# Performance work log

Hardware: AMD Instinct MI355X
Metric: run time of the kernel (lower is better)

The kernel has to match this reference:

```python
import jax, jax.numpy as jnp
import numpy as np

D, VH, DFF, NL, VOCAB, NH, NKV, HD, R, SCALE = 4096, 1024, 14336, 2, 32000, 32, 8, 128, 8, 4.0
B, NIMG, T = 2, 257, 511
S = NIMG + T

def _rmsnorm(x, w, eps=1e-5):
    v = jnp.mean(jnp.square(x), axis=-1, keepdims=True)
    return x * jax.lax.rsqrt(v + eps) * w

def _lora(x, W, A, Bm):
    # base (dequantized NF4 equivalent) matmul + low-rank LoRA path, scaling = alpha/r
    base = jnp.einsum('...d,od->...o', x, W)
    low = jnp.einsum('...r,or->...o', jnp.einsum('...d,rd->...r', x, A), Bm)
    return base + low * SCALE

def _rope_tables(s):
    inv = 1.0 / (10000.0 ** (jnp.arange(0, HD, 2, dtype=jnp.float32) / HD))
    ang = jnp.arange(s, dtype=jnp.float32)[:, None] * inv[None, :]
    c, sn = jnp.cos(ang), jnp.sin(ang)
    return jnp.concatenate([c, c], -1), jnp.concatenate([sn, sn], -1)

def _apply_rope(x, cos, sin):
    rot = jnp.concatenate([-x[..., HD // 2:], x[..., :HD // 2]], -1)
    return x * cos + rot * sin

def _forward(image_embeds, proj_W, proj_b, embed, ln1, ln2, ln_f, Wq, Aq, Bq, Wk, Ak, Bk, Wv, Av, Bv, Wo, Ao, Bo, Wg, Ag, Bg, Wu, Au, Bu, Wd, Ad, Bd, input_ids, attention_mask):
    b = image_embeds.shape[0]
    img = jnp.einsum('bsv,dv->bsd', image_embeds, proj_W) + proj_b  # projector
    txt = embed[input_ids]                                          # token embedding lookup
    h = jnp.concatenate([img, txt], axis=1)                         # (B, S, D)
    s = h.shape[1]
    cos, sin = _rope_tables(s)
    allow = jnp.tril(jnp.ones((s, s), bool))[None, None] & (attention_mask[:, None, None, :] > 0)
    for i in range(NL):
        x = _rmsnorm(h, ln1[i])
        q = _lora(x, Wq[i], Aq[i], Bq[i]).reshape(b, s, NH, HD).transpose(0, 2, 1, 3)
        k = _lora(x, Wk[i], Ak[i], Bk[i]).reshape(b, s, NKV, HD).transpose(0, 2, 1, 3)
        v = _lora(x, Wv[i], Av[i], Bv[i]).reshape(b, s, NKV, HD).transpose(0, 2, 1, 3)
        q = _apply_rope(q, cos, sin)
        k = _apply_rope(k, cos, sin)
        k = jnp.repeat(k, NH // NKV, axis=1)  # GQA: expand kv heads
        v = jnp.repeat(v, NH // NKV, axis=1)
        scores = jnp.einsum('bhsd,bhtd->bhst', q, k) / jnp.sqrt(jnp.float32(HD))
        scores = jnp.where(allow, scores, jnp.float32(-1e30))
        attn = jnp.einsum('bhst,bhtd->bhsd', jax.nn.softmax(scores, axis=-1), v)
        attn = attn.transpose(0, 2, 1, 3).reshape(b, s, D)
        h = h + _lora(attn, Wo[i], Ao[i], Bo[i])
        x = _rmsnorm(h, ln2[i])
        h = h + _lora(jax.nn.silu(_lora(x, Wg[i], Ag[i], Bg[i])) * _lora(x, Wu[i], Au[i], Bu[i]), Wd[i], Ad[i], Bd[i])
    return _rmsnorm(h, ln_f)  # HF hidden_states[-1] is post final norm

def setup_inputs():
    key = jax.random.key(0)
    ks = iter(jax.random.split(key, 40))
    n = lambda shape, sc=0.02: jax.random.normal(next(ks), shape, jnp.float32) * sc
    return dict(
        image_embeds=jax.random.normal(next(ks), (B, NIMG, VH), jnp.float32),
        input_ids=jax.random.randint(next(ks), (B, T), 0, VOCAB),
        attention_mask=jnp.ones((B, S), jnp.int32),
        proj_W=n((D, VH)), proj_b=jnp.zeros((D,), jnp.float32),
        embed=n((VOCAB, D)),
        ln1=jnp.ones((NL, D), jnp.float32), ln2=jnp.ones((NL, D), jnp.float32), ln_f=jnp.ones((D,), jnp.float32),
        Wq=n((NL, D, D)), Aq=n((NL, R, D)), Bq=n((NL, D, R)),
        Wk=n((NL, NKV * HD, D)), Ak=n((NL, R, D)), Bk=n((NL, NKV * HD, R)),
        Wv=n((NL, NKV * HD, D)), Av=n((NL, R, D)), Bv=n((NL, NKV * HD, R)),
        Wo=n((NL, D, D)), Ao=n((NL, R, D)), Bo=n((NL, D, R)),
        Wg=n((NL, DFF, D)), Ag=n((NL, R, D)), Bg=n((NL, DFF, R)),
        Wu=n((NL, DFF, D)), Au=n((NL, R, D)), Bu=n((NL, DFF, R)),
        Wd=n((NL, D, DFF)), Ad=n((NL, R, DFF)), Bd=n((NL, D, R)),
    )

def reference(image_embeds, input_ids, attention_mask, proj_W, proj_b, embed, ln1, ln2, ln_f, Wq, Aq, Bq, Wk, Ak, Bk, Wv, Av, Bv, Wo, Ao, Bo, Wg, Ag, Bg, Wu, Au, Bu, Wd, Ad, Bd):
    return _forward(image_embeds, proj_W, proj_b, embed, ln1, ln2, ln_f, Wq, Aq, Bq, Wk, Ak, Bk, Wv, Av, Bv, Wo, Ao, Bo, Wg, Ag, Bg, Wu, Au, Bu, Wd, Ad, Bd, input_ids, attention_mask)
```

## Files before the change

kernel.cpp:

```cpp
#include <hip/hip_runtime.h>
#include <hip/hip_bf16.h>
#include <cstdint>
#include <cstddef>

typedef unsigned short u16;
typedef unsigned int u32;
typedef __attribute__((ext_vector_type(8))) short short8;
typedef __attribute__((ext_vector_type(4))) short short4v;
typedef __attribute__((ext_vector_type(4))) float f32x4;

__device__ __forceinline__ u16 f2bf(float f) {
  u32 u = __float_as_uint(f);
  u32 r = (u + 0x7FFFu + ((u >> 16) & 1u)) >> 16;
  return (u16)r;
}
__device__ __forceinline__ float bf2f(u16 u) {
  return __uint_as_float(((u32)u) << 16);
}
__device__ __forceinline__ short f2bf_hw(float f) {
  union { __hip_bfloat16 h; u16 u; } c;
  c.h = __float2bfloat16(f);
  return (short)c.u;
}

__device__ __forceinline__ void gload_lds16(const void* g, void* l) {
  __builtin_amdgcn_global_load_lds((const __attribute__((address_space(1))) void*)g,
                                   (__attribute__((address_space(3))) void*)l, 16, 0, 0);
}

__global__ __launch_bounds__(256) void convert_w_kernel(const float* __restrict__ src,
    u16* __restrict__ dst, long n8) {
  long stride = (long)gridDim.x * 256;
  for (long i = (long)blockIdx.x * 256 + threadIdx.x; i < n8; i += stride) {
    const float* p = src + i * 8;
    float4 v0 = *(const float4*)p;
    float4 v1 = *(const float4*)(p + 4);
    uint4 w;
    w.x = (u32)(u16)f2bf_hw(v0.x) | ((u32)(u16)f2bf_hw(v0.y) << 16);
    w.y = (u32)(u16)f2bf_hw(v0.z) | ((u32)(u16)f2bf_hw(v0.w) << 16);
    w.z = (u32)(u16)f2bf_hw(v1.x) | ((u32)(u16)f2bf_hw(v1.y) << 16);
    w.w = (u32)(u16)f2bf_hw(v1.z) | ((u32)(u16)f2bf_hw(v1.w) << 16);
    *(uint4*)(dst + i * 8) = w;
  }
}

struct ConvJob { const float* src; u16* dst; long n8; };
struct GemmArgs {
  const u16* A; int M; int K; int lda;
  const float* W0; const float* LB0; int toff0;
  const float* W1; const float* LB1; int toff1;
  const float* W2; const float* LB2; int toff2;
  const u16* Wb0; const u16* Wb1; const u16* Wb2;
  int ldw;
  int seg1; int seg2;
  const float* t;
  const float* bias;
  const float* resid;
  float* outf; int ostride;
  u16* outb0; u16* outb1;
  int rowremap;
  float* outp;
  int ny_main;
  ConvJob cj[3];
};

template<int WMODE>
__global__ __launch_bounds__(256) void gemm_kernel(GemmArgs a) {
  __shared__ u16 Asm[128 * 64];
  __shared__ u16 BsmW[WMODE ? 128 * 64 : 128 * 128];
  const int tid = threadIdx.x;

  const int nconv = (int)gridDim.y - a.ny_main;
  if ((int)blockIdx.y < nconv) {
    if (blockIdx.z != 0) return;
    const long cb = (long)blockIdx.y * gridDim.x + blockIdx.x;
    const long cstr = (long)nconv * gridDim.x * 256;
#pragma unroll
    for (int j = 0; j < 3; j++) {
      const float* src = a.cj[j].src;
      if (!src) break;
      u16* dst = a.cj[j].dst;
      const long n8 = a.cj[j].n8;
      for (long i = cb * 256 + tid; i < n8; i += cstr) {
        const float* p = src + i * 8;
        float4 v0 = *(const float4*)p;
        float4 v1 = *(const float4*)(p + 4);
        uint4 w;
        w.x = (u32)(u16)f2bf_hw(v0.x) | ((u32)(u16)f2bf_hw(v0.y) << 16);
        w.y = (u32)(u16)f2bf_hw(v0.z) | ((u32)(u16)f2bf_hw(v0.w) << 16);
        w.z = (u32)(u16)f2bf_hw(v1.x) | ((u32)(u16)f2bf_hw(v1.y) << 16);
        w.w = (u32)(u16)f2bf_hw(v1.z) | ((u32)(u16)f2bf_hw(v1.w) << 16);
        *(uint4*)(dst + i * 8) = w;
      }
    }
    return;
  }
  const int yid = (int)blockIdx.y - nconv;

  const int nwg = gridDim.x * a.ny_main;
  const int bid0 = yid * gridDim.x + blockIdx.x;
  const int q = nwg >> 3, r = nwg & 7;
  const int xcd = bid0 & 7, pos = bid0 >> 3;
  const int nb = (xcd < r ? xcd * (q + 1) : r * (q + 1) + (xcd - r) * q) + pos;
  const int m0 = (nb % gridDim.x) * 128;
  const int n0 = (nb / gridDim.x) * 128;

  const float* W = a.W0; const u16* Wb = a.Wb0;
  const float* LB = a.LB0; int toff = a.toff0; int nbase = 0;
  if (a.seg2 && n0 >= a.seg2)      { W = a.W2; Wb = a.Wb2; LB = a.LB2; toff = a.toff2; nbase = a.seg2; }
  else if (a.seg1 && n0 >= a.seg1) { W = a.W1; Wb = a.Wb1; LB = a.LB1; toff = a.toff1; nbase = a.seg1; }
  const int koff = blockIdx.z * a.K;
  const u16* Ab = a.A + koff;
  const float* Wt = W + (size_t)(n0 - nbase) * a.ldw + koff;
  const u16* Wbt = Wb + (size_t)(n0 - nbase) * a.ldw + koff;

  const int lane = tid & 63, wid = tid >> 6;
  const int wr = wid >> 1, wcn = wid & 1;
  const int lrow = lane & 15, g = lane >> 4;
  const int arow = lane >> 3;
  const int aslot = (lane & 7) ^ arow;
  const int brow4 = lane >> 4;

  f32x4 acc[4][4] = {};

  auto dma_A = [&](int k0) {
#pragma unroll
    for (int i = 0; i < 4; i++) {
      int c = wid * 4 + i;
      const u16* src = Ab + (size_t)(m0 + c * 8 + arow) * a.lda + k0 + (aslot << 3);
      gload_lds16(src, &Asm[c * 512]);
    }
  };
  auto dma_B = [&](int k0) {
    if (WMODE) {
#pragma unroll
      for (int i = 0; i < 4; i++) {
        int c = wid * 4 + i;
        const u16* src = Wbt + (size_t)(c * 8 + arow) * a.ldw + k0 + (aslot << 3);
        gload_lds16(src, &BsmW[c * 512]);
      }
    } else {
      float* Bf = (float*)BsmW;
#pragma unroll
      for (int j = 0; j < 8; j++) {
        int rrow = wid * 32 + j * 4 + brow4;
        int sslot = (lane & 15) ^ (rrow & 7);
        const float* src = Wt + (size_t)rrow * a.ldw + k0 + (sslot << 2);
        gload_lds16(src, &Bf[(wid * 32 + j * 4) * 64]);
      }
    }
  };

  dma_A(0);
  dma_B(0);
  const int nk = a.K >> 6;
  for (int kt = 0; kt < nk; kt++) {
    __syncthreads();

    short8 af[4][2], bq[4][2];
#pragma unroll
    for (int mi = 0; mi < 4; mi++) {
      int row = wr * 64 + mi * 16 + lrow;
#pragma unroll
      for (int x = 0; x < 2; x++) {
        int s = x * 4 + g;
        af[mi][x] = *(const short8*)&Asm[row * 64 + ((s ^ (lrow & 7)) << 3)];
      }
    }
#pragma unroll
    for (int ni = 0; ni < 4; ni++) {
      int row = wcn * 64 + ni * 16 + lrow;
      if (WMODE) {
#pragma unroll
        for (int x = 0; x < 2; x++) {
          int s = x * 4 + g;
          bq[ni][x] = *(const short8*)&BsmW[row * 64 + ((s ^ (lrow & 7)) << 3)];
        }
      } else {
        const float* bp = (const float*)BsmW + row * 64;
        int m = row & 7;
#pragma unroll
        for (int x = 0; x < 2; x++) {
          int sg0 = x * 8 + g * 2;
          f32x4 lo = *(const f32x4*)(bp + ((sg0 ^ m) << 2));
          f32x4 hi = *(const f32x4*)(bp + (((sg0 + 1) ^ m) << 2));
          short8 sv;
          sv[0] = f2bf_hw(lo[0]); sv[1] = f2bf_hw(lo[1]);
          sv[2] = f2bf_hw(lo[2]); sv[3] = f2bf_hw(lo[3]);
          sv[4] = f2bf_hw(hi[0]); sv[5] = f2bf_hw(hi[1]);
          sv[6] = f2bf_hw(hi[2]); sv[7] = f2bf_hw(hi[3]);
          bq[ni][x] = sv;
        }
      }
    }

    asm volatile("s_waitcnt lgkmcnt(0)" ::: "memory");
    __builtin_amdgcn_sched_barrier(0);
    __builtin_amdgcn_s_barrier();
    __builtin_amdgcn_sched_barrier(0);
    if (kt + 1 < nk) {
      dma_A((kt + 1) << 6);
      dma_B((kt + 1) << 6);
    }
#pragma unroll
    for (int x = 0; x < 2; x++)
#pragma unroll
      for (int mi = 0; mi < 4; mi++)
#pragma unroll
        for (int ni = 0; ni < 4; ni++)
          acc[mi][ni] = __builtin_amdgcn_mfma_f32_16x16x32_bf16(af[mi][x], bq[ni][x], acc[mi][ni], 0, 0, 0);
  }

  if (a.outp) {
    float* op = a.outp + (size_t)blockIdx.z * (1536 * 4096);
#pragma unroll
    for (int mi = 0; mi < 4; mi++)
#pragma unroll
      for (int rr = 0; rr < 4; rr++) {
        int row = m0 + wr * 64 + mi * 16 + (g << 2) + rr;
#pragma unroll
        for (int ni = 0; ni < 4; ni++) {
          int n = n0 + wcn * 64 + ni * 16 + lrow;
          op[(size_t)row * a.ostride + n] = acc[mi][ni][rr];
        }
      }
    return;
  }
  const bool dolora = (a.t != nullptr);
  float lbv[4][8];
#pragma unroll
  for (int ni = 0; ni < 4; ni++) {
    if (dolora) {
      int cl = wcn * 64 + ni * 16 + lrow;
      const float* bp = LB + (size_t)(n0 - nbase + cl) * 8;
#pragma unroll
      for (int r2 = 0; r2 < 8; r2++) lbv[ni][r2] = bp[r2];
    }
  }
#pragma unroll
  for (int mi = 0; mi < 4; mi++) {
#pragma unroll
    for (int rr = 0; rr < 4; rr++) {
      int row = m0 + wr * 64 + mi * 16 + (g << 2) + rr;
      if (row >= a.M) continue;
      float tv[8];
      if (dolora) {
        const float* tp = a.t + row * 32 + toff;
#pragma unroll
        for (int r2 = 0; r2 < 8; r2++) tv[r2] = tp[r2];
      }
#pragma unroll
      for (int ni = 0; ni < 4; ni++) {
        int n = n0 + wcn * 64 + ni * 16 + lrow;
        float val = acc[mi][ni][rr];
        if (dolora) {
          float ds = 0.f;
#pragma unroll
          for (int r2 = 0; r2 < 8; r2++) ds += tv[r2] * lbv[ni][r2];
          val += 4.0f * ds;
        }
        if (a.bias)  val += a.bias[n];
        if (a.resid) val += a.resid[(size_t)row * 4096 + n];
        if (a.outf) {
          int orow = a.rowremap ? (row < 257 ? row : row + 511) : row;
          a.outf[(size_t)orow * a.ostride + n] = val;
        } else if (a.seg1 && n >= a.seg1) {
          a.outb1[(size_t)row * a.ostride + (n - a.seg1)] = f2bf(val);
        } else {
          a.outb0[(size_t)row * a.ostride + n] = f2bf(val);
        }
      }
    }
  }
}

__global__ __launch_bounds__(256) void combine_kernel(float* __restrict__ h,
    const float* __restrict__ p, const float* __restrict__ t,
    const float* __restrict__ LB) {
  const int row = blockIdx.x;
  float tv[8];
  const float* tp = t + row * 32;
#pragma unroll
  for (int r = 0; r < 8; r++) tv[r] = tp[r];
  const float* p1 = p + (size_t)1536 * 4096;
#pragma unroll
  for (int i = 0; i < 4; i++) {
    int base = threadIdx.x * 4 + i * 1024;
    size_t off = (size_t)row * 4096 + base;
    float4 hv = *(const float4*)(h + off);
    float4 a0 = *(const float4*)(p + off);
    float4 a1 = *(const float4*)(p1 + off);
    float o[4] = {hv.x + a0.x + a1.x, hv.y + a0.y + a1.y,
                  hv.z + a0.z + a1.z, hv.w + a0.w + a1.w};
#pragma unroll
    for (int j = 0; j < 4; j++) {
      const float* lb = LB + (size_t)(base + j) * 8;
      float ds = 0.f;
#pragma unroll
      for (int r = 0; r < 8; r++) ds += tv[r] * lb[r];
      o[j] += 4.0f * ds;
    }
    float4 ov; ov.x = o[0]; ov.y = o[1]; ov.z = o[2]; ov.w = o[3];
    *(float4*)(h + off) = ov;
  }
}

template<int NA>
__global__ __launch_bounds__(256) void lora_xa_kernel(const u16* __restrict__ X, int K,
    const float* A0, const float* A1, const float* A2, float* __restrict__ t) {
  const int m = blockIdx.x;
  const u16* xr = X + (size_t)m * K;
  float acc[NA * 8];
#pragma unroll
  for (int i = 0; i < NA * 8; i++) acc[i] = 0.f;
  const float* Ap[3] = {A0, A1, A2};
  for (int k = threadIdx.x * 8; k < K; k += 2048) {
    uint4 xv = *(const uint4*)(xr + k);
    float xf[8];
    xf[0] = bf2f((u16)(xv.x & 0xffff)); xf[1] = bf2f((u16)(xv.x >> 16));
    xf[2] = bf2f((u16)(xv.y & 0xffff)); xf[3] = bf2f((u16)(xv.y >> 16));
    xf[4] = bf2f((u16)(xv.z & 0xffff)); xf[5] = bf2f((u16)(xv.z >> 16));
    xf[6] = bf2f((u16)(xv.w & 0xffff)); xf[7] = bf2f((u16)(xv.w >> 16));
#pragma unroll
    for (int aa = 0; aa < NA; aa++) {
#pragma unroll
      for (int r = 0; r < 8; r++) {
        const float* ar = Ap[aa] + (size_t)r * K + k;
        float4 a0 = *(const float4*)ar;
        float4 a1 = *(const float4*)(ar + 4);
        acc[aa * 8 + r] += xf[0] * a0.x + xf[1] * a0.y + xf[2] * a0.z + xf[3] * a0.w
                         + xf[4] * a1.x + xf[5] * a1.y + xf[6] * a1.z + xf[7] * a1.w;
      }
    }
  }
  __shared__ float red[4][NA * 8];
#pragma unroll
  for (int i = 0; i < NA * 8; i++) {
    float v = acc[i];
#pragma unroll
    for (int o = 1; o < 64; o <<= 1) v += __shfl_xor(v, o);
    if ((threadIdx.x & 63) == 0) red[threadIdx.x >> 6][i] = v;
  }
  __syncthreads();
  if (threadIdx.x < NA * 8)
    t[m * 32 + threadIdx.x] = red[0][threadIdx.x] + red[1][threadIdx.x]
                            + red[2][threadIdx.x] + red[3][threadIdx.x];
}

__global__ __launch_bounds__(256) void rmsnorm_kernel(const float* __restrict__ h,
    const float* __restrict__ w, u16* outb, float* outf) {
  const int m = blockIdx.x;
  const float* row = h + (size_t)m * 4096;
  float4 v[4];
  float ss = 0.f;
#pragma unroll
  for (int i = 0; i < 4; i++) {
    v[i] = *(const float4*)(row + threadIdx.x * 4 + i * 1024);
    ss += v[i].x * v[i].x + v[i].y * v[i].y + v[i].z * v[i].z + v[i].w * v[i].w;
  }
#pragma unroll
  for (int o = 1; o < 64; o <<= 1) ss += __shfl_xor(ss, o);
  __shared__ float red[4];
  if ((threadIdx.x & 63) == 0) red[threadIdx.x >> 6] = ss;
  __syncthreads();
  ss = red[0] + red[1] + red[2] + red[3];
  float rs = rsqrtf(ss * (1.f / 4096.f) + 1e-5f);
#pragma unroll
  for (int i = 0; i < 4; i++) {
    int base = threadIdx.x * 4 + i * 1024;
    float4 wv = *(const float4*)(w + base);
    float o0 = v[i].x * rs * wv.x, o1 = v[i].y * rs * wv.y;
    float o2 = v[i].z * rs * wv.z, o3 = v[i].w * rs * wv.w;
    if (outb) {
      short4v sv; sv.x = (short)f2bf(o0); sv.y = (short)f2bf(o1);
      sv.z = (short)f2bf(o2); sv.w = (short)f2bf(o3);
      *(short4v*)(outb + (size_t)m * 4096 + base) = sv;
    } else {
      float4 ov; ov.x = o0; ov.y = o1; ov.z = o2; ov.w = o3;
      *(float4*)(outf + (size_t)m * 4096 + base) = ov;
    }
  }
}

__global__ void rope_tab_kernel(float2* __restrict__ tab) {
  int idx = blockIdx.x * 256 + threadIdx.x;
  int s = idx >> 6, i = idx & 63;
  float inv = __expf(-(float)i * (9.210340371976184f / 64.f));
  float ang = (float)s * inv;
  float sn, cs;
  sincosf(ang, &sn, &cs);
  float2 r; r.x = cs; r.y = sn;
  tab[idx] = r;
}

__global__ __launch_bounds__(256) void rope_apply_kernel(float* __restrict__ qkv,
    const float2* __restrict__ tab) {
  int m = blockIdx.x;
  int s = m % 768;
  float* rowp = qkv + (size_t)m * 6144;
  for (int idx = threadIdx.x; idx < 2560; idx += 256) {
    int head = idx >> 6, i = idx & 63;
    int col = (head < 32) ? head * 128 : 4096 + (head - 32) * 128;
    float2 cs = tab[s * 64 + i];
    float x0 = rowp[col + i], x1 = rowp[col + i + 64];
    rowp[col + i]      = x0 * cs.x - x1 * cs.y;
    rowp[col + i + 64] = x1 * cs.x + x0 * cs.y;
  }
}

__global__ __launch_bounds__(256) void attn_mfma_kernel(const float* __restrict__ qkv,
    const int* __restrict__ amask, u16* __restrict__ attn_bf) {
  __shared__ u16 Ks[4][32][40];
  __shared__ u16 Vt[128][40];
  __shared__ u16 Ps[4][16][40];
  const int b = blockIdx.z, hh = blockIdx.y, q0 = blockIdx.x * 64;
  const int kvh = hh >> 2;
  const int tid = threadIdx.x, lane = tid & 63, w = tid >> 6;
  const int lrow = lane & 15, g = lane >> 4;
  const float sc = 0.08838834764831845f;

  short8 qf[4];
  {
    const float* qp = qkv + ((size_t)(b * 768 + q0 + w * 16 + lrow)) * 6144 + hh * 128;
#pragma unroll
    for (int ks = 0; ks < 4; ks++) {
      float4 lo = *(const float4*)(qp + ks * 32 + g * 8);
      float4 hi = *(const float4*)(qp + ks * 32 + g * 8 + 4);
      short8 sv;
      sv[0] = f2bf_hw(lo.x * sc); sv[1] = f2bf_hw(lo.y * sc);
      sv[2] = f2bf_hw(lo.z * sc); sv[3] = f2bf_hw(lo.w * sc);
      sv[4] = f2bf_hw(hi.x * sc); sv[5] = f2bf_hw(hi.y * sc);
      sv[6] = f2bf_hw(hi.z * sc); sv[7] = f2bf_hw(hi.w * sc);
      qf[ks] = sv;
    }
  }

  f32x4 acco[8] = {};
  float mrun[4] = {-1e30f, -1e30f, -1e30f, -1e30f};
  float lrun[4] = {0.f, 0.f, 0.f, 0.f};
  const int ntile = (q0 >> 5) + 2;

  for (int kt = 0; kt < ntile; kt++) {
    const int k0 = kt * 32;
    __syncthreads();
#pragma unroll
    for (int i = 0; i < 4; i++) {
      int idx = i * 256 + tid;
      int r2 = idx >> 5, c4 = (idx & 31) << 2;
      const float* kp = qkv + ((size_t)(b * 768 + k0 + r2)) * 6144 + 4096 + kvh * 128 + c4;
      float4 kv = *(const float4*)kp;
      short4v ksv;
      ksv.x = f2bf_hw(kv.x); ksv.y = f2bf_hw(kv.y);
      ksv.z = f2bf_hw(kv.z); ksv.w = f2bf_hw(kv.w);
      *(short4v*)&Ks[c4 >> 5][r2][c4 & 31] = ksv;
      float4 vv = *(const float4*)(kp + 1024);
      Vt[c4 + 0][r2] = (u16)f2bf_hw(vv.x);
      Vt[c4 + 1][r2] = (u16)f2bf_hw(vv.y);
      Vt[c4 + 2][r2] = (u16)f2bf_hw(vv.z);
      Vt[c4 + 3][r2] = (u16)f2bf_hw(vv.w);
    }
    __syncthreads();

    f32x4 s0 = {}, s1 = {};
#pragma unroll
    for (int ks = 0; ks < 4; ks++) {
      short8 kb0 = *(const short8*)&Ks[ks][lrow][g * 8];
      short8 kb1 = *(const short8*)&Ks[ks][16 + lrow][g * 8];
      s0 = __builtin_amdgcn_mfma_f32_16x16x32_bf16(qf[ks], kb0, s0, 0, 0, 0);
      s1 = __builtin_amdgcn_mfma_f32_16x16x32_bf16(qf[ks], kb1, s1, 0, 0, 0);
    }
    const int key0 = k0 + lrow, key1 = k0 + 16 + lrow;
    const bool am0 = amask[b * 768 + key0] != 0;
    const bool am1 = amask[b * 768 + key1] != 0;
    float scl4[4];
#pragma unroll
    for (int rr = 0; rr < 4; rr++) {
      int qrow = q0 + w * 16 + g * 4 + rr;
      float v0 = (key0 <= qrow && am0) ? s0[rr] : -1e30f;
      float v1 = (key1 <= qrow && am1) ? s1[rr] : -1e30f;
      float m = fmaxf(v0, v1);
      m = fmaxf(m, __shfl_xor(m, 1));
      m = fmaxf(m, __shfl_xor(m, 2));
      m = fmaxf(m, __shfl_xor(m, 4));
      m = fmaxf(m, __shfl_xor(m, 8));
      float mnew = fmaxf(mrun[rr], m);
      float scl = __expf(mrun[rr] - mnew);
      float p0 = __expf(v0 - mnew);
      float p1 = __expf(v1 - mnew);
      float ls = p0 + p1;
      ls += __shfl_xor(ls, 1);
      ls += __shfl_xor(ls, 2);
      ls += __shfl_xor(ls, 4);
      ls += __shfl_xor(ls, 8);
      lrun[rr] = lrun[rr] * scl + ls;
      mrun[rr] = mnew;
      scl4[rr] = scl;
      Ps[w][g * 4 + rr][lrow]      = (u16)f2bf_hw(p0);
      Ps[w][g * 4 + rr][16 + lrow] = (u16)f2bf_hw(p1);
    }
#pragma unroll
    for (int nf = 0; nf < 8; nf++)
#pragma unroll
      for (int rr = 0; rr < 4; rr++) acco[nf][rr] *= scl4[rr];

    asm volatile("s_waitcnt lgkmcnt(0)" ::: "memory");
    __builtin_amdgcn_sched_barrier(0);
    short8 pa = *(const short8*)&Ps[w][lrow][g * 8];
#pragma unroll
    for (int nf = 0; nf < 8; nf++) {
      short8 vb = *(const short8*)&Vt[nf * 16 + lrow][g * 8];
      acco[nf] = __builtin_amdgcn_mfma_f32_16x16x32_bf16(pa, vb, acco[nf], 0, 0, 0);
    }
  }

#pragma unroll
  for (int rr = 0; rr < 4; rr++) {
    float inv = 1.f / lrun[rr];
    size_t orow = (size_t)(b * 768 + q0 + w * 16 + g * 4 + rr);
#pragma unroll
    for (int nf = 0; nf < 8; nf++)
      attn_bf[orow * 4096 + hh * 128 + nf * 16 + lrow] = f2bf(acco[nf][rr] * inv);
  }
}

__global__ void convert_img_kernel(const float* __restrict__ in, u16* __restrict__ out) {
  int idx = blockIdx.x * 256 + threadIdx.x;
  if (idx >= 81920) return;
  uint4 w = {0u, 0u, 0u, 0u};
  if (idx < 65792) {
    const float* p = in + (size_t)idx * 8;
    float4 v0 = *(const float4*)p;
    float4 v1 = *(const float4*)(p + 4);
    w.x = (u32)f2bf(v0.x) | ((u32)f2bf(v0.y) << 16);
    w.y = (u32)f2bf(v0.z) | ((u32)f2bf(v0.w) << 16);
    w.z = (u32)f2bf(v1.x) | ((u32)f2bf(v1.y) << 16);
    w.w = (u32)f2bf(v1.z) | ((u32)f2bf(v1.w) << 16);
  }
  *(uint4*)(out + (size_t)idx * 8) = w;
}

__global__ void embed_gather_kernel(const float* __restrict__ embed,
    const int* __restrict__ ids, float* __restrict__ h) {
  int row = blockIdx.x;
  int b = row / 511, tt = row % 511;
  int id = ids[b * 511 + tt];
  const float* src = embed + (size_t)id * 4096;
  float* dst = h + ((size_t)(b * 768 + 257 + tt)) * 4096;
  for (int i = threadIdx.x * 4; i < 4096; i += 1024)
    *(float4*)(dst + i) = *(const float4*)(src + i);
}

__global__ __launch_bounds__(256) void gu_combine_kernel(const u16* __restrict__ g,
    const u16* __restrict__ u, u16* __restrict__ x2) {
  size_t idx = (size_t)blockIdx.x * 256 + threadIdx.x;
  uint4 gv = *(const uint4*)(g + idx * 8);
  uint4 uv = *(const uint4*)(u + idx * 8);
  u32 gi[4] = {gv.x, gv.y, gv.z, gv.w};
  u32 ui[4] = {uv.x, uv.y, uv.z, uv.w};
  u32 oi[4];
#pragma unroll
  for (int i = 0; i < 4; i++) {
    float g0 = bf2f((u16)(gi[i] & 0xffff)), g1 = bf2f((u16)(gi[i] >> 16));
    float u0 = bf2f((u16)(ui[i] & 0xffff)), u1 = bf2f((u16)(ui[i] >> 16));
    float s0 = g0 / (1.f + __expf(-g0)) * u0;
    float s1 = g1 / (1.f + __expf(-g1)) * u1;
    oi[i] = (u32)f2bf(s0) | ((u32)f2bf(s1) << 16);
  }
  uint4 ov; ov.x = oi[0]; ov.y = oi[1]; ov.z = oi[2]; ov.w = oi[3];
  *(uint4*)(x2 + idx * 8) = ov;
}

extern "C" void kernel_launch(void* const* d_in, const int* in_sizes, int n_in,
                              void* d_out, int out_size, void* d_ws, size_t ws_size,
                              hipStream_t stream) {
  const float* image_embeds = (const float*)d_in[0];
  const int*   input_ids    = (const int*)d_in[1];
  const int*   amask        = (const int*)d_in[2];
  const float* proj_W = (const float*)d_in[3];
  const float* proj_b = (const float*)d_in[4];
  const float* embed  = (const float*)d_in[5];
  const float* ln1 = (const float*)d_in[6];
  const float* ln2 = (const float*)d_in[7];
  const float* ln_f = (const float*)d_in[8];
  const float* Wq = (const float*)d_in[9];
  const float* Aq = (const float*)d_in[10];
  const float* Bq = (const float*)d_in[11];
  const float* Wk = (const float*)d_in[12];
  const float* Ak = (const float*)d_in[13];
  const float* Bk = (const float*)d_in[14];
  const float* Wv = (const float*)d_in[15];
  const float* Av = (const float*)d_in[16];
  const float* Bv = (const float*)d_in[17];
  const float* Wo = (const float*)d_in[18];
  const float* Ao = (const float*)d_in[19];
  const float* Bo = (const float*)d_in[20];
  const float* Wg = (const float*)d_in[21];
  const float* Ag = (const float*)d_in[22];
  const float* Bg = (const float*)d_in[23];
  const float* Wu = (const float*)d_in[24];
  const float* Au = (const float*)d_in[25];
  const float* Bu = (const float*)d_in[26];
  const float* Wd = (const float*)d_in[27];
  const float* Ad = (const float*)d_in[28];
  const float* Bd = (const float*)d_in[29];
  (void)in_sizes; (void)n_in; (void)out_size;

  char* ws = (char*)d_ws;
  size_t off = 0;
  auto alloc = [&](size_t bytes) -> void* {
    void* p = ws + off; off += (bytes + 255) & ~(size_t)255; return p;
  };
  float* h       = (float*) alloc((size_t)1536 * 4096 * 4);
  u16*   xn      = (u16*)   alloc((size_t)1536 * 4096 * 2);
  float* qkv     = (float*) alloc((size_t)1536 * 6144 * 4);
  u16*   attn_bf = (u16*)   alloc((size_t)1536 * 4096 * 2);
  u16*   g_bf    = (u16*)   alloc((size_t)1536 * 14336 * 2);
  u16*   u_bf    = (u16*)   alloc((size_t)1536 * 14336 * 2);
  u16*   x2_bf   = (u16*)   alloc((size_t)1536 * 14336 * 2);
  float* t       = (float*) alloc((size_t)1536 * 32 * 4);
  float2* tab    = (float2*)alloc((size_t)768 * 64 * 8);
  u16*   img_bf  = (u16*)   alloc((size_t)640 * 1024 * 2);
  float* pc      = (float*) alloc((size_t)2 * 1536 * 4096 * 4);
  const size_t nQ = (size_t)2 * 4096 * 4096;
  const size_t nK = (size_t)2 * 1024 * 4096;
  const size_t nG = (size_t)2 * 14336 * 4096;
  const long nQl8 = 4096L * 4096 / 8, nKl8 = 1024L * 4096 / 8, nGl8 = 14336L * 4096 / 8;
  u16* wq_b = (u16*)alloc(nQ * 2);
  u16* wk_b = (u16*)alloc(nK * 2);
  u16* wv_b = (u16*)alloc(nK * 2);
  u16* wo_b = (u16*)alloc(nQ * 2);
  u16* wg_b = (u16*)alloc(nG * 2);
  u16* wu_b = (u16*)alloc(nG * 2);
  u16* wd_b = (u16*)alloc(nG * 2);
  const bool use_bf = (off <= ws_size);
  const int CONVY = 16;

  dim3 blk(256);
  if (use_bf) {
    convert_w_kernel<<<dim3(512), blk, 0, stream>>>(Wq, wq_b, nQl8);
    convert_w_kernel<<<dim3(256), blk, 0, stream>>>(Wk, wk_b, nKl8);
    convert_w_kernel<<<dim3(256), blk, 0, stream>>>(Wv, wv_b, nKl8);
  }
  auto launch_gemm = [&](const GemmArgs& a, dim3 grid) {
    if (a.Wb0) gemm_kernel<1><<<grid, blk, 0, stream>>>(a);
    else       gemm_kernel<0><<<grid, blk, 0, stream>>>(a);
  };

  convert_img_kernel<<<dim3(320), blk, 0, stream>>>(image_embeds, img_bf);
  rope_tab_kernel<<<dim3(192), blk, 0, stream>>>(tab);

  {
    GemmArgs a = {};
    a.A = img_bf; a.M = 514; a.K = 1024; a.lda = 1024; a.ldw = 1024;
    a.W0 = proj_W;
    a.bias = proj_b;
    a.outf = h; a.ostride = 4096; a.rowremap = 1;
    a.ny_main = 32;
    launch_gemm(a, dim3(5, 32));
  }
  embed_gather_kernel<<<dim3(1022), blk, 0, stream>>>(embed, input_ids, h);

  for (int l = 0; l < 2; l++) {
    const float* Wq_l = Wq + (size_t)l * 4096 * 4096;
    const float* Aq_l = Aq + (size_t)l * 8 * 4096;
    const float* Bq_l = Bq + (size_t)l * 4096 * 8;
    const float* Wk_l = Wk + (size_t)l * 1024 * 4096;
    const float* Ak_l = Ak + (size_t)l * 8 * 4096;
    const float* Bk_l = Bk + (size_t)l * 1024 * 8;
    const float* Wv_l = Wv + (size_t)l * 1024 * 4096;
    const float* Av_l = Av + (size_t)l * 8 * 4096;
    const float* Bv_l = Bv + (size_t)l * 1024 * 8;
    const float* Wo_l = Wo + (size_t)l * 4096 * 4096;
    const float* Ao_l = Ao + (size_t)l * 8 * 4096;
    const float* Bo_l = Bo + (size_t)l * 4096 * 8;
    const float* Wg_l = Wg + (size_t)l * 14336 * 4096;
    const float* Ag_l = Ag + (size_t)l * 8 * 4096;
    const float* Bg_l = Bg + (size_t)l * 14336 * 8;
    const float* Wu_l = Wu + (size_t)l * 14336 * 4096;
    const float* Au_l = Au + (size_t)l * 8 * 4096;
    const float* Bu_l = Bu + (size_t)l * 14336 * 8;
    const float* Wd_l = Wd + (size_t)l * 4096 * 14336;
    const float* Ad_l = Ad + (size_t)l * 8 * 14336;
    const float* Bd_l = Bd + (size_t)l * 4096 * 8;
    u16* wq_bl = wq_b + (size_t)l * 4096 * 4096;
    u16* wk_bl = wk_b + (size_t)l * 1024 * 4096;
    u16* wv_bl = wv_b + (size_t)l * 1024 * 4096;
    u16* wo_bl = wo_b + (size_t)l * 4096 * 4096;
    u16* wg_bl = wg_b + (size_t)l * 14336 * 4096;
    u16* wu_bl = wu_b + (size_t)l * 14336 * 4096;
    u16* wd_bl = wd_b + (size_t)l * 14336 * 4096;

    rmsnorm_kernel<<<dim3(1536), blk, 0, stream>>>(h, ln1 + l * 4096, xn, (float*)nullptr);
    lora_xa_kernel<3><<<dim3(1536), blk, 0, stream>>>(xn, 4096, Aq_l, Ak_l, Av_l, t);
    {
      GemmArgs a = {};
      a.A = xn; a.M = 1536; a.K = 4096; a.lda = 4096; a.ldw = 4096;
      a.W0 = Wq_l; a.LB0 = Bq_l; a.toff0 = 0;
      a.W1 = Wk_l; a.LB1 = Bk_l; a.toff1 = 8;
      a.W2 = Wv_l; a.LB2 = Bv_l; a.toff2 = 16;
      a.seg1 = 4096; a.seg2 = 5120;
      a.t = t; a.outf = qkv; a.ostride = 6144;
      a.ny_main = 48;
      dim3 grid(12, 48);
      if (use_bf) {
        a.Wb0 = wq_bl; a.Wb1 = wk_bl; a.Wb2 = wv_bl;
        a.cj[0] = {Wo_l, wo_bl, nQl8};
        a.cj[1] = {Wg_l, wg_bl, nGl8};
        grid = dim3(12, 48 + CONVY);
      }
      launch_gemm(a, grid);
    }
    rope_apply_kernel<<<dim3(1536), blk, 0, stream>>>(qkv, tab);
    attn_mfma_kernel<<<dim3(12, 32, 2), blk, 0, stream>>>(qkv, amask, attn_bf);
    lora_xa_kernel<1><<<dim3(1536), blk, 0, stream>>>(attn_bf, 4096, Ao_l,
        (const float*)nullptr, (const float*)nullptr, t);
    {
      GemmArgs a = {};
      a.A = attn_bf; a.M = 1536; a.K = 2048; a.lda = 4096; a.ldw = 4096;
      a.W0 = Wo_l;
      a.ostride = 4096; a.outp = pc;
      a.ny_main = 32;
      dim3 grid(12, 32, 2);
      if (use_bf) {
        a.Wb0 = wo_bl;
        a.cj[0] = {Wu_l, wu_bl, nGl8};
        grid = dim3(12, 32 + CONVY, 2);
      }
      launch_gemm(a, grid);
      combine_kernel<<<dim3(1536), blk, 0, stream>>>(h, pc, t, Bo_l);
    }
    rmsnorm_kernel<<<dim3(1536), blk, 0, stream>>>(h, ln2 + l * 4096, xn, (float*)nullptr);
    lora_xa_kernel<2><<<dim3(1536), blk, 0, stream>>>(xn, 4096, Ag_l, Au_l,
        (const float*)nullptr, t);
    {
      GemmArgs a = {};
      a.A = xn; a.M = 1536; a.K = 4096; a.lda = 4096; a.ldw = 4096;
      a.W0 = Wg_l; a.LB0 = Bg_l; a.toff0 = 0;
      a.W1 = Wu_l; a.LB1 = Bu_l; a.toff1 = 8;
      a.seg1 = 14336;
      a.t = t; a.outb0 = g_bf; a.outb1 = u_bf; a.ostride = 14336;
      a.ny_main = 224;
      dim3 grid(12, 224);
      if (use_bf) {
        a.Wb0 = wg_bl; a.Wb1 = wu_bl;
        a.cj[0] = {Wd_l, wd_bl, nGl8};
        grid = dim3(12, 224 + CONVY);
      }
      launch_gemm(a, grid);
    }
    gu_combine_kernel<<<dim3(10752), blk, 0, stream>>>(g_bf, u_bf, x2_bf);
    lora_xa_kernel<1><<<dim3(1536), blk, 0, stream>>>(x2_bf, 14336, Ad_l,
        (const float*)nullptr, (const float*)nullptr, t);
    {
      GemmArgs a = {};
      a.A = x2_bf; a.M = 1536; a.K = 7168; a.lda = 14336; a.ldw = 14336;
      a.W0 = Wd_l;
      a.ostride = 4096; a.outp = pc;
      a.ny_main = 32;
      dim3 grid(12, 32, 2);
      if (use_bf) {
        a.Wb0 = wd_bl;
        if (l == 0) {
          a.cj[0] = {Wq + (size_t)4096 * 4096, wq_b + (size_t)4096 * 4096, nQl8};
          a.cj[1] = {Wk + (size_t)1024 * 4096, wk_b + (size_t)1024 * 4096, nKl8};
          a.cj[2] = {Wv + (size_t)1024 * 4096, wv_b + (size_t)1024 * 4096, nKl8};
          grid = dim3(12, 32 + CONVY, 2);
        }
      }
      launch_gemm(a, grid);
      combine_kernel<<<dim3(1536), blk, 0, stream>>>(h, pc, t, Bd_l);
    }
  }
  rmsnorm_kernel<<<dim3(1536), blk, 0, stream>>>(h, ln_f, (u16*)nullptr, (float*)d_out);
}
```

Measured before the change: 3.040 ms.

## Double-buffer GEMM shared-memory tiles to prefetch two K-steps ahead

Splits the A and B shared-memory tiles into two buffers and issues the global-to-LDS loads for tile k+2 while tile k is consumed. Partial vmcnt waits replace the full __syncthreads at the top of the loop. The aim is to hide global load latency behind the MFMA work. In exchange, LDS use per block doubles, up to 96KB in the fp32-weight mode, which can cut occupancy. The hard-coded vmcnt counts must exactly match the number of outstanding loads per tile, or the kernel races.

```diff
diff --git a/kernel.cpp b/kernel.cpp
--- a/kernel.cpp
+++ b/kernel.cpp
@@ -66,8 +66,8 @@
 
 template<int WMODE>
 __global__ __launch_bounds__(256) void gemm_kernel(GemmArgs a) {
-  __shared__ u16 Asm[128 * 64];
-  __shared__ u16 BsmW[WMODE ? 128 * 64 : 128 * 128];
+  __shared__ u16 Asm[2][128 * 64];
+  __shared__ u16 BsmW[2][WMODE ? 128 * 64 : 128 * 128];
   const int tid = threadIdx.x;
 
   const int nconv = (int)gridDim.y - a.ny_main;
@@ -123,24 +123,24 @@
 
   f32x4 acc[4][4] = {};
 
-  auto dma_A = [&](int k0) {
+  auto dma_A = [&](int k0, int buf) {
 #pragma unroll
     for (int i = 0; i < 4; i++) {
       int c = wid * 4 + i;
       const u16* src = Ab + (size_t)(m0 + c * 8 + arow) * a.lda + k0 + (aslot << 3);
-      gload_lds16(src, &Asm[c * 512]);
+      gload_lds16(src, &Asm[buf][c * 512]);
     }
   };
-  auto dma_B = [&](int k0) {
+  auto dma_B = [&](int k0, int buf) {
     if (WMODE) {
 #pragma unroll
       for (int i = 0; i < 4; i++) {
         int c = wid * 4 + i;
         const u16* src = Wbt + (size_t)(c * 8 + arow) * a.ldw + k0 + (aslot << 3);
-        gload_lds16(src, &BsmW[c * 512]);
+        gload_lds16(src, &BsmW[buf][c * 512]);
       }
     } else {
-      float* Bf = (float*)BsmW;
+      float* Bf = (float*)&BsmW[buf][0];
 #pragma unroll
       for (int j = 0; j < 8; j++) {
         int rrow = wid * 32 + j * 4 + brow4;
@@ -151,11 +151,21 @@
     }
   };
 
-  dma_A(0);
-  dma_B(0);
   const int nk = a.K >> 6;
+  dma_A(0, 0); dma_B(0, 0);
+  if (nk > 1) { dma_A(64, 1); dma_B(64, 1); }
+
   for (int kt = 0; kt < nk; kt++) {
-    __syncthreads();
+    const int cur = kt & 1;
+    if (kt + 1 < nk) {
+      if (WMODE) asm volatile("s_waitcnt vmcnt(8)" ::: "memory");
+      else       asm volatile("s_waitcnt vmcnt(12)" ::: "memory");
+    } else {
+      asm volatile("s_waitcnt vmcnt(0)" ::: "memory");
+    }
+    __builtin_amdgcn_sched_barrier(0);
+    __builtin_amdgcn_s_barrier();
+    __builtin_amdgcn_sched_barrier(0);
 
     short8 af[4][2], bq[4][2];
 #pragma unroll
@@ -164,7 +174,7 @@
 #pragma unroll
       for (int x = 0; x < 2; x++) {
         int s = x * 4 + g;
-        af[mi][x] = *(const short8*)&Asm[row * 64 + ((s ^ (lrow & 7)) << 3)];
+        af[mi][x] = *(const short8*)&Asm[cur][row * 64 + ((s ^ (lrow & 7)) << 3)];
       }
     }
 #pragma unroll
@@ -174,10 +184,10 @@
 #pragma unroll
         for (int x = 0; x < 2; x++) {
           int s = x * 4 + g;
-          bq[ni][x] = *(const short8*)&BsmW[row * 64 + ((s ^ (lrow & 7)) << 3)];
+          bq[ni][x] = *(const short8*)&BsmW[cur][row * 64 + ((s ^ (lrow & 7)) << 3)];
         }
       } else {
-        const float* bp = (const float*)BsmW + row * 64;
+        const float* bp = (const float*)&BsmW[cur][0] + row * 64;
         int m = row & 7;
 #pragma unroll
         for (int x = 0; x < 2; x++) {
@@ -198,10 +208,11 @@
     __builtin_amdgcn_sched_barrier(0);
     __builtin_amdgcn_s_barrier();
     __builtin_amdgcn_sched_barrier(0);
-    if (kt + 1 < nk) {
-      dma_A((kt + 1) << 6);
-      dma_B((kt + 1) << 6);
-    }
+    if (kt + 2 < nk) {
+      dma_A((kt + 2) << 6, cur);
+      dma_B((kt + 2) << 6, cur);
+    }
+    __builtin_amdgcn_sched_barrier(0);
 #pragma unroll
     for (int x = 0; x < 2; x++)
 #pragma unroll
```

Result: no change. 3.043 ms (+0.1%).

## Process two K-subtiles per barrier in bf16-weight GEMM path

Applied to the files above, without the earlier changes.

For the bf16-weight GEMM mode, the K loop now stages two 64-wide K slices into separate LDS halves and handles 128 of K per iteration. Each pair of slices needs one vmcnt wait and two barriers, and the MFMAs on the first half run while the second half's fragments are read. The aim is to halve the synchronisation and load-issue overhead per unit of K and to issue larger DMA batches. The cost is doubled LDS (A and B buffers both grow to 32KB), which may reduce occupancy, and K must be a multiple of 128.

```diff
diff --git a/kernel.cpp b/kernel.cpp
--- a/kernel.cpp
+++ b/kernel.cpp
@@ -66,8 +66,8 @@
 
 template<int WMODE>
 __global__ __launch_bounds__(256) void gemm_kernel(GemmArgs a) {
-  __shared__ u16 Asm[128 * 64];
-  __shared__ u16 BsmW[WMODE ? 128 * 64 : 128 * 128];
+  __shared__ u16 Asm[16384];
+  __shared__ u16 BsmW[16384];
   const int tid = threadIdx.x;
 
   const int nconv = (int)gridDim.y - a.ny_main;
@@ -123,60 +123,126 @@
 
   f32x4 acc[4][4] = {};
 
-  auto dma_A = [&](int k0) {
+  auto dma_A = [&](int k0, int half) {
 #pragma unroll
     for (int i = 0; i < 4; i++) {
       int c = wid * 4 + i;
       const u16* src = Ab + (size_t)(m0 + c * 8 + arow) * a.lda + k0 + (aslot << 3);
-      gload_lds16(src, &Asm[c * 512]);
+      gload_lds16(src, &Asm[half * 8192 + c * 512]);
     }
   };
-  auto dma_B = [&](int k0) {
-    if (WMODE) {
-#pragma unroll
-      for (int i = 0; i < 4; i++) {
-        int c = wid * 4 + i;
-        const u16* src = Wbt + (size_t)(c * 8 + arow) * a.ldw + k0 + (aslot << 3);
-        gload_lds16(src, &BsmW[c * 512]);
-      }
-    } else {
-      float* Bf = (float*)BsmW;
-#pragma unroll
-      for (int j = 0; j < 8; j++) {
-        int rrow = wid * 32 + j * 4 + brow4;
-        int sslot = (lane & 15) ^ (rrow & 7);
-        const float* src = Wt + (size_t)rrow * a.ldw + k0 + (sslot << 2);
-        gload_lds16(src, &Bf[(wid * 32 + j * 4) * 64]);
-      }
+  auto dma_B1 = [&](int k0, int half) {
+#pragma unroll
+    for (int i = 0; i < 4; i++) {
+      int c = wid * 4 + i;
+      const u16* src = Wbt + (size_t)(c * 8 + arow) * a.ldw + k0 + (aslot << 3);
+      gload_lds16(src, &BsmW[half * 8192 + c * 512]);
     }
   };
-
-  dma_A(0);
-  dma_B(0);
-  const int nk = a.K >> 6;
-  for (int kt = 0; kt < nk; kt++) {
-    __syncthreads();
-
-    short8 af[4][2], bq[4][2];
-#pragma unroll
-    for (int mi = 0; mi < 4; mi++) {
-      int row = wr * 64 + mi * 16 + lrow;
-#pragma unroll
-      for (int x = 0; x < 2; x++) {
-        int s = x * 4 + g;
-        af[mi][x] = *(const short8*)&Asm[row * 64 + ((s ^ (lrow & 7)) << 3)];
-      }
-    }
-#pragma unroll
-    for (int ni = 0; ni < 4; ni++) {
-      int row = wcn * 64 + ni * 16 + lrow;
-      if (WMODE) {
+  auto dma_B0 = [&](int k0) {
+    float* Bf = (float*)BsmW;
+#pragma unroll
+    for (int j = 0; j < 8; j++) {
+      int rrow = wid * 32 + j * 4 + brow4;
+      int sslot = (lane & 15) ^ (rrow & 7);
+      const float* src = Wt + (size_t)rrow * a.ldw + k0 + (sslot << 2);
+      gload_lds16(src, &Bf[(wid * 32 + j * 4) * 64]);
+    }
+  };
+
+  if (WMODE) {
+    const int nk = a.K >> 7;
+    dma_A(0, 0); dma_B1(0, 0);
+    dma_A(64, 1); dma_B1(64, 1);
+    for (int kt = 0; kt < nk; kt++) {
+      const int k0 = kt << 7;
+      asm volatile("s_waitcnt vmcnt(0)" ::: "memory");
+      __builtin_amdgcn_sched_barrier(0);
+      __builtin_amdgcn_s_barrier();
+      __builtin_amdgcn_sched_barrier(0);
+      {
+        short8 af[4][2], bq[4][2];
+#pragma unroll
+        for (int mi = 0; mi < 4; mi++) {
+          int row = wr * 64 + mi * 16 + lrow;
+#pragma unroll
+          for (int x = 0; x < 2; x++) {
+            int s = x * 4 + g;
+            af[mi][x] = *(const short8*)&Asm[row * 64 + ((s ^ (lrow & 7)) << 3)];
+          }
+        }
+#pragma unroll
+        for (int ni = 0; ni < 4; ni++) {
+          int row = wcn * 64 + ni * 16 + lrow;
+#pragma unroll
+          for (int x = 0; x < 2; x++) {
+            int s = x * 4 + g;
+            bq[ni][x] = *(const short8*)&BsmW[row * 64 + ((s ^ (lrow & 7)) << 3)];
+          }
+        }
+#pragma unroll
+        for (int x = 0; x < 2; x++)
+#pragma unroll
+          for (int mi = 0; mi < 4; mi++)
+#pragma unroll
+            for (int ni = 0; ni < 4; ni++)
+              acc[mi][ni] = __builtin_amdgcn_mfma_f32_16x16x32_bf16(af[mi][x], bq[ni][x], acc[mi][ni], 0, 0, 0);
+      }
+      short8 af1[4][2], bq1[4][2];
+#pragma unroll
+      for (int mi = 0; mi < 4; mi++) {
+        int row = wr * 64 + mi * 16 + lrow;
 #pragma unroll
         for (int x = 0; x < 2; x++) {
           int s = x * 4 + g;
-          bq[ni][x] = *(const short8*)&BsmW[row * 64 + ((s ^ (lrow & 7)) << 3)];
-        }
-      } else {
+          af1[mi][x] = *(const short8*)&Asm[8192 + row * 64 + ((s ^ (lrow & 7)) << 3)];
+        }
+      }
+#pragma unroll
+      for (int ni = 0; ni < 4; ni++) {
+        int row = wcn * 64 + ni * 16 + lrow;
+#pragma unroll
+        for (int x = 0; x < 2; x++) {
+          int s = x * 4 + g;
+          bq1[ni][x] = *(const short8*)&BsmW[8192 + row * 64 + ((s ^ (lrow & 7)) << 3)];
+        }
+      }
+      asm volatile("s_waitcnt lgkmcnt(0)" ::: "memory");
+      __builtin_amdgcn_sched_barrier(0);
+      __builtin_amdgcn_s_barrier();
+      __builtin_amdgcn_sched_barrier(0);
+      if (kt + 1 < nk) {
+        dma_A(k0 + 128, 0); dma_B1(k0 + 128, 0);
+        dma_A(k0 + 192, 1); dma_B1(k0 + 192, 1);
+      }
+      __builtin_amdgcn_sched_barrier(0);
+#pragma unroll
+      for (int x = 0; x < 2; x++)
+#pragma unroll
+        for (int mi = 0; mi < 4; mi++)
+#pragma unroll
+          for (int ni = 0; ni < 4; ni++)
+            acc[mi][ni] = __builtin_amdgcn_mfma_f32_16x16x32_bf16(af1[mi][x], bq1[ni][x], acc[mi][ni], 0, 0, 0);
+    }
+  } else {
+    const int nk = a.K >> 6;
+    dma_A(0, 0);
+    dma_B0(0);
+    for (int kt = 0; kt < nk; kt++) {
+      __syncthreads();
+      short8 af[4][2], bq[4][2];
+#pragma unroll
+      for (int mi = 0; mi < 4; mi++) {
+        int row = wr * 64 + mi * 16 + lrow;
+#pragma unroll
+        for (int x = 0; x < 2; x++) {
+          int s = x * 4 + g;
+          af[mi][x] = *(const short8*)&Asm[row * 64 + ((s ^ (lrow & 7)) << 3)];
+        }
+      }
+#pragma unroll
+      for (int ni = 0; ni < 4; ni++) {
+        int row = wcn * 64 + ni * 16 + lrow;
         const float* bp = (const float*)BsmW + row * 64;
         int m = row & 7;
 #pragma unroll
@@ -192,23 +258,22 @@
           bq[ni][x] = sv;
         }
       }
-    }
-
-    asm volatile("s_waitcnt lgkmcnt(0)" ::: "memory");
-    __builtin_amdgcn_sched_barrier(0);
-    __builtin_amdgcn_s_barrier();
-    __builtin_amdgcn_sched_barrier(0);
-    if (kt + 1 < nk) {
-      dma_A((kt + 1) << 6);
-      dma_B((kt + 1) << 6);
-    }
-#pragma unroll
-    for (int x = 0; x < 2; x++)
-#pragma unroll
-      for (int mi = 0; mi < 4; mi++)
-#pragma unroll
-        for (int ni = 0; ni < 4; ni++)
-          acc[mi][ni] = __builtin_amdgcn_mfma_f32_16x16x32_bf16(af[mi][x], bq[ni][x], acc[mi][ni], 0, 0, 0);
+      asm volatile("s_waitcnt lgkmcnt(0)" ::: "memory");
+      __builtin_amdgcn_sched_barrier(0);
+      __builtin_amdgcn_s_barrier();
+      __builtin_amdgcn_sched_barrier(0);
+      if (kt + 1 < nk) {
+        dma_A((kt + 1) << 6, 0);
+        dma_B0((kt + 1) << 6);
+      }
+#pragma unroll
+      for (int x = 0; x < 2; x++)
+#pragma unroll
+        for (int mi = 0; mi < 4; mi++)
+#pragma unroll
+          for (int ni = 0; ni < 4; ni++)
+            acc[mi][ni] = __builtin_amdgcn_mfma_f32_16x16x32_bf16(af[mi][x], bq[ni][x], acc[mi][ni], 0, 0, 0);
+    }
   }
 
   if (a.outp) {
```

Result: slower. 3.128 ms (+2.9%).
